# Optimization experiments

Hardware: AMD Instinct MI355X
Metric: run time of the kernel (lower is better)

The kernel has to match this reference:

```python
import jax, jax.numpy as jnp
import numpy as np

N_HEADS = 16
HEAD_DIM = 64
D_MODEL = N_HEADS * HEAD_DIM
NEG_INF = -10000.0


def setup_inputs() -> dict:
    key = jax.random.key(0)
    ks = jax.random.split(key, 6)
    B, S = 2, 2048
    std = 0.02
    return {
        "from_tensor": jax.random.normal(ks[0], (B, S, D_MODEL), dtype=jnp.float32),
        "to_tensor": jax.random.normal(ks[1], (B, S, D_MODEL), dtype=jnp.float32),
        "attention_mask": jnp.ones((B, S, S), dtype=jnp.int32),
        "Wq": jax.random.normal(ks[2], (D_MODEL, D_MODEL), dtype=jnp.float32) * std,
        "bq": jnp.zeros((D_MODEL,), dtype=jnp.float32),
        "Wk": jax.random.normal(ks[3], (D_MODEL, D_MODEL), dtype=jnp.float32) * std,
        "bk": jnp.zeros((D_MODEL,), dtype=jnp.float32),
        "Wv": jax.random.normal(ks[4], (D_MODEL, D_MODEL), dtype=jnp.float32) * std,
        "bv": jnp.zeros((D_MODEL,), dtype=jnp.float32),
    }


def reference(from_tensor, to_tensor, attention_mask, Wq, bq, Wk, bk, Wv, bv):
    B, F, _ = from_tensor.shape
    T = to_tensor.shape[1]
    # Dense QKV projections (no activation by default)
    q = from_tensor @ Wq + bq          # [B, F, N*H]
    k = to_tensor @ Wk + bk            # [B, T, N*H]
    v = to_tensor @ Wv + bv            # [B, T, N*H]
    # split heads -> [B, N, S, H]
    q = q.reshape(B, F, N_HEADS, HEAD_DIM).transpose(0, 2, 1, 3)
    k = k.reshape(B, T, N_HEADS, HEAD_DIM).transpose(0, 2, 1, 3)
    v = v.reshape(B, T, N_HEADS, HEAD_DIM).transpose(0, 2, 1, 3)
    # scaled dot-product scores [B, N, F, T]
    scores = jnp.einsum("bnfh,bnth->bnft", q, k) / jnp.sqrt(jnp.float32(HEAD_DIM))
    # additive mask: (1 - mask) * -10000, broadcast over heads
    adder = (1.0 - attention_mask.astype(jnp.float32))[:, None, :, :] * NEG_INF
    scores = scores + adder
    probs = jax.nn.softmax(scores, axis=-1)  # dropout is identity at inference
    ctx = jnp.einsum("bnft,bnth->bnfh", probs, v)  # [B, N, F, H]
    return ctx.transpose(0, 2, 1, 3).reshape(B, F, N_HEADS * HEAD_DIM)
```

## Files before the change

### kernel.cpp

```cpp
#include <hip/hip_runtime.h>
#include <hip/hip_bf16.h>

typedef unsigned short u16;
typedef __bf16 bf16x8 __attribute__((ext_vector_type(8)));
typedef float f32x4 __attribute__((ext_vector_type(4)));

#define D_MODEL 1024
#define NH 16
#define HD 64
#define SEQ 2048
#define BATCH 2

__device__ __forceinline__ f32x4 mfma16(bf16x8 a, bf16x8 b, f32x4 c) {
    return __builtin_amdgcn_mfma_f32_16x16x32_bf16(a, b, c, 0, 0, 0);
}

__device__ __forceinline__ u16 f2bf(float f) {
    __hip_bfloat16 h = __float2bfloat16(f);
    return *reinterpret_cast<u16*>(&h);
}

__device__ __forceinline__ void gload_lds16(const void* g, void* l) {
    __builtin_amdgcn_global_load_lds((__attribute__((address_space(1))) void*)g,
                                     (__attribute__((address_space(3))) void*)l,
                                     16, 0, 0);
}

__global__ __launch_bounds__(256) void convert_k(const float* __restrict__ src,
                                                 u16* __restrict__ dst, int n8) {
    const int i = blockIdx.x * 256 + threadIdx.x;
    if (i >= n8) return;
    const float4 a = ((const float4*)src)[i * 2];
    const float4 b = ((const float4*)src)[i * 2 + 1];
    union { u16 h[8]; uint4 v; } u;
    u.h[0] = f2bf(a.x); u.h[1] = f2bf(a.y); u.h[2] = f2bf(a.z); u.h[3] = f2bf(a.w);
    u.h[4] = f2bf(b.x); u.h[5] = f2bf(b.y); u.h[6] = f2bf(b.z); u.h[7] = f2bf(b.w);
    *(uint4*)(dst + i * 8) = u.v;
}

__global__ __launch_bounds__(256) void transposeW_k(const float* __restrict__ src,
                                                    u16* __restrict__ dst,
                                                    int R, int C) {
    __shared__ __align__(16) u16 t[64][72];
    const int tid = threadIdx.x;
    const int r0 = blockIdx.y * 64, c0 = blockIdx.x * 64;
#pragma unroll
    for (int j = 0; j < 2; ++j) {
        int idx = j * 256 + tid;
        int rr = idx >> 3, cc = idx & 7;
        size_t base = (size_t)(r0 + rr) * C + c0 + cc * 8;
        float4 a = *(const float4*)(src + base);
        float4 b = *(const float4*)(src + base + 4);
        union { u16 h[8]; uint4 v; } u;
        u.h[0] = f2bf(a.x); u.h[1] = f2bf(a.y); u.h[2] = f2bf(a.z); u.h[3] = f2bf(a.w);
        u.h[4] = f2bf(b.x); u.h[5] = f2bf(b.y); u.h[6] = f2bf(b.z); u.h[7] = f2bf(b.w);
        *(uint4*)&t[rr][cc * 8] = u.v;
    }
    __syncthreads();
#pragma unroll
    for (int j = 0; j < 2; ++j) {
        int idx = j * 256 + tid;
        int cc = idx >> 3, rr8 = idx & 7;
        union { u16 h[8]; uint4 v; } u;
#pragma unroll
        for (int e = 0; e < 8; ++e) u.h[e] = t[rr8 * 8 + e][cc];
        *(uint4*)(dst + (size_t)(c0 + cc) * R + r0 + rr8 * 8) = u.v;
    }
}

__global__ __launch_bounds__(256) void maskflags_k(const int* __restrict__ mask,
                                                   int* __restrict__ flags) {
    const int tid = threadIdx.x;
    const int ti = blockIdx.x, fi = blockIdx.y, b = blockIdx.z;
    const int f = fi * 128 + (tid >> 1);
    const int4* p = (const int4*)(mask + ((size_t)(b * SEQ + f)) * SEQ + ti * 64 + (tid & 1) * 32);
    int ok = 1;
#pragma unroll
    for (int j = 0; j < 8; ++j) {
        int4 v = p[j];
        ok &= (v.x == 1) & (v.y == 1) & (v.z == 1) & (v.w == 1);
    }
    __shared__ int sflag;
    if (tid == 0) sflag = 1;
    __syncthreads();
    if (!ok) sflag = 0;
    __syncthreads();
    if (tid == 0) flags[(b * 16 + fi) * 32 + ti] = sflag;
}

__global__ __launch_bounds__(256, 2) void qkv_gemm_k(
    const u16* __restrict__ Xq, const u16* __restrict__ Xkv,
    const u16* __restrict__ Wt,
    const float* __restrict__ bq, const float* __restrict__ bk,
    const float* __restrict__ bv,
    u16* __restrict__ Qb, u16* __restrict__ Kb, u16* __restrict__ Vt) {
    const int z = blockIdx.z;
    const u16* X = (z == 0) ? Xq : Xkv;
    const u16* Wz = Wt + (size_t)z * D_MODEL * D_MODEL;
    const float* bias = (z == 0) ? bq : (z == 1 ? bk : bv);
    const float scale = (z == 0) ? 0.1803368801111244f : 1.0f;

    __shared__ __align__(16) u16 As[128 * 32];
    __shared__ __align__(16) u16 Bs[128 * 32];

    const int tid = threadIdx.x;
    const int w = tid >> 6, lane = tid & 63;
    const int q = lane >> 4, c = lane & 15;
    const int m0 = blockIdx.x * 128, n0 = blockIdx.y * 128;
    const int mw = (w & 1) * 64, nw = (w >> 1) * 64;

    f32x4 acc[4][4];
    const f32x4 z4 = {0.f, 0.f, 0.f, 0.f};
#pragma unroll
    for (int mi = 0; mi < 4; ++mi)
#pragma unroll
        for (int ni = 0; ni < 4; ++ni) acc[mi][ni] = z4;

    for (int kb = 0; kb < 32; ++kb) {
        const int k0 = kb * 32;
#pragma unroll
        for (int j = 0; j < 2; ++j) {
            int i = j * 256 + tid;
            int r = i >> 2, cc = i & 3;
            gload_lds16(X + (size_t)(m0 + r) * D_MODEL + k0 + cc * 8, As + i * 8);
            gload_lds16(Wz + (size_t)(n0 + r) * D_MODEL + k0 + cc * 8, Bs + i * 8);
        }
        __syncthreads();
        bf16x8 af[4], bfr[4];
#pragma unroll
        for (int mi = 0; mi < 4; ++mi)
            af[mi] = *(const bf16x8*)(As + (mw + mi * 16 + c) * 32 + q * 8);
#pragma unroll
        for (int ni = 0; ni < 4; ++ni)
            bfr[ni] = *(const bf16x8*)(Bs + (nw + ni * 16 + c) * 32 + q * 8);
#pragma unroll
        for (int mi = 0; mi < 4; ++mi)
#pragma unroll
            for (int ni = 0; ni < 4; ++ni)
                acc[mi][ni] = mfma16(af[mi], bfr[ni], acc[mi][ni]);
        __syncthreads();
    }

    if (z == 2) {
#pragma unroll
        for (int ni = 0; ni < 4; ++ni) {
            const int colg = n0 + nw + ni * 16 + c;
            const float bvv = bias[colg];
            const int head = colg >> 6, h = colg & 63;
#pragma unroll
            for (int mi = 0; mi < 4; ++mi) {
                const int rowg = m0 + mw + mi * 16 + q * 4;
                const int b = rowg >> 11, s = rowg & 2047;
                union { u16 h4[4]; uint2 v2; } pk;
#pragma unroll
                for (int r = 0; r < 4; ++r) pk.h4[r] = f2bf(acc[mi][ni][r] + bvv);
                *(uint2*)(Vt + (((size_t)(b * NH + head)) * HD + h) * SEQ + s) = pk.v2;
            }
        }
    } else {
        u16* outb = (z == 0) ? Qb : Kb;
#pragma unroll
        for (int ni = 0; ni < 4; ++ni) {
            const int colg = n0 + nw + ni * 16 + c;
            const float bvv = bias[colg];
            const int head = colg >> 6, h = colg & 63;
#pragma unroll
            for (int mi = 0; mi < 4; ++mi) {
                const int rowg = m0 + mw + mi * 16 + q * 4;
#pragma unroll
                for (int r = 0; r < 4; ++r) {
                    const int mrow = rowg + r;
                    const int b = mrow >> 11, s = mrow & 2047;
                    const float val = (acc[mi][ni][r] + bvv) * scale;
                    outb[(((size_t)(b * NH + head)) * SEQ + s) * HD + h] = f2bf(val);
                }
            }
        }
    }
}

#define SK_OFF (128 * 144)
#define SV_OFF (SK_OFF + 64 * 144)
#define SMEM_BYTES (SV_OFF + 64 * 144)

__global__ __launch_bounds__(256, 4) void attn_k(
    const u16* __restrict__ Qb, const u16* __restrict__ Kb, const u16* __restrict__ Vt,
    const int* __restrict__ flags, const int* __restrict__ mask,
    float* __restrict__ out) {
    __shared__ __align__(16) unsigned char smem[SMEM_BYTES];
    const int tid = threadIdx.x;
    const int w = tid >> 6, lane = tid & 63;
    const int q = lane >> 4, c = lane & 15;
    const int fi = blockIdx.x, bn = blockIdx.y;
    const int b = bn >> 4, n = bn & 15;
    const int f0 = fi * 128;

    u16* sQ = (u16*)(smem);
    u16* sK = (u16*)(smem + SK_OFF);
    u16* sV = (u16*)(smem + SV_OFF);
    u16* sP = sQ + w * 32 * 72;

#pragma unroll
    for (int j = 0; j < 4; ++j) {
        int i = j * 256 + tid;
        int r = i >> 3, cc = i & 7;
        uint4 v = *(const uint4*)(Qb + ((size_t)(bn * SEQ + f0 + r)) * HD + cc * 8);
        *(uint4*)(sQ + r * 72 + cc * 8) = v;
    }
    __syncthreads();

    bf16x8 qf[2][2];
#pragma unroll
    for (int ft = 0; ft < 2; ++ft)
#pragma unroll
        for (int kb = 0; kb < 2; ++kb)
            qf[ft][kb] = *(const bf16x8*)(sQ + (w * 32 + ft * 16 + c) * 72 + kb * 32 + q * 8);
    __asm__ __volatile__("" ::: "memory");
    __builtin_amdgcn_s_waitcnt(0xC07F);
    __asm__ __volatile__("" ::: "memory");

    union { u16 h[8]; bf16x8 v; } one_u;
#pragma unroll
    for (int j = 0; j < 8; ++j) one_u.h[j] = 0x3F80;
    const bf16x8 ones = one_u.v;

    f32x4 O[2][4], accL[2];
    const f32x4 z4 = {0.f, 0.f, 0.f, 0.f};
#pragma unroll
    for (int mi = 0; mi < 2; ++mi) {
        accL[mi] = z4;
#pragma unroll
        for (int hi = 0; hi < 4; ++hi) O[mi][hi] = z4;
    }
    const int* flagp = flags + (b * 16 + fi) * 32;

    for (int it = 0; it < 32; ++it) {
        const int t0 = it * 64;
#pragma unroll
        for (int j = 0; j < 2; ++j) {
            int i = j * 256 + tid;
            int r = i >> 3, cc = i & 7;
            uint4 kv = *(const uint4*)(Kb + ((size_t)(bn * SEQ + t0 + r)) * HD + cc * 8);
            uint4 vv = *(const uint4*)(Vt + ((size_t)(bn * HD + r)) * SEQ + t0 + cc * 8);
            *(uint4*)(sK + r * 72 + cc * 8) = kv;
            *(uint4*)(sV + r * 72 + cc * 8) = vv;
        }
        __syncthreads();

        const int maskslow = (flagp[it] == 0);

#pragma unroll
        for (int mt = 0; mt < 4; ++mt) {
            bf16x8 kf0 = *(const bf16x8*)(sK + (mt * 16 + c) * 72 + 0 + q * 8);
            bf16x8 kf1 = *(const bf16x8*)(sK + (mt * 16 + c) * 72 + 32 + q * 8);
            f32x4 st[2];
#pragma unroll
            for (int ft = 0; ft < 2; ++ft) {
                st[ft] = z4;
                st[ft] = mfma16(kf0, qf[ft][0], st[ft]);
                st[ft] = mfma16(kf1, qf[ft][1], st[ft]);
            }
            if (maskslow) {
#pragma unroll
                for (int ft = 0; ft < 2; ++ft)
#pragma unroll
                    for (int r = 0; r < 4; ++r) {
                        const int fg = f0 + w * 32 + ft * 16 + c;
                        const int tg = t0 + mt * 16 + q * 4 + r;
                        const int mv = mask[((size_t)(b * SEQ + fg)) * SEQ + tg];
                        st[ft][r] += (1.0f - (float)mv) * (-10000.0f) * 1.4426950408889634f;
                    }
            }
#pragma unroll
            for (int ft = 0; ft < 2; ++ft) {
                union { u16 h[4]; uint2 v2; } pk;
#pragma unroll
                for (int r = 0; r < 4; ++r)
                    pk.h[r] = f2bf(exp2f(st[ft][r] - 10.0f));
                *(uint2*)(sP + (ft * 16 + c) * 72 + mt * 16 + q * 4) = pk.v2;
            }
        }
        __asm__ __volatile__("" ::: "memory");
        __builtin_amdgcn_s_waitcnt(0xC07F);
        __asm__ __volatile__("" ::: "memory");

#pragma unroll
        for (int kb = 0; kb < 2; ++kb) {
            bf16x8 pf0 = *(const bf16x8*)(sP + (0 * 16 + c) * 72 + kb * 32 + q * 8);
            bf16x8 pf1 = *(const bf16x8*)(sP + (1 * 16 + c) * 72 + kb * 32 + q * 8);
#pragma unroll
            for (int hi = 0; hi < 4; ++hi) {
                bf16x8 vf = *(const bf16x8*)(sV + (hi * 16 + c) * 72 + kb * 32 + q * 8);
                O[0][hi] = mfma16(pf0, vf, O[0][hi]);
                O[1][hi] = mfma16(pf1, vf, O[1][hi]);
            }
            accL[0] = mfma16(pf0, ones, accL[0]);
            accL[1] = mfma16(pf1, ones, accL[1]);
        }
        __syncthreads();
    }

    float linv[2][4];
#pragma unroll
    for (int mi = 0; mi < 2; ++mi)
#pragma unroll
        for (int r = 0; r < 4; ++r) linv[mi][r] = 1.0f / accL[mi][r];
#pragma unroll
    for (int mi = 0; mi < 2; ++mi)
#pragma unroll
        for (int hi = 0; hi < 4; ++hi)
#pragma unroll
            for (int r = 0; r < 4; ++r) {
                const int fg = f0 + w * 32 + mi * 16 + q * 4 + r;
                const int col = n * 64 + hi * 16 + c;
                out[((size_t)(b * SEQ + fg)) * D_MODEL + col] = O[mi][hi][r] * linv[mi][r];
            }
}

__global__ __launch_bounds__(256) void signal_k(float* __restrict__ out, int n,
                                                float val) {
    const int i = blockIdx.x * 256 + threadIdx.x;
    if (i < n) out[i] = val;
}

extern "C" void kernel_launch(void* const* d_in, const int* in_sizes, int n_in,
                              void* d_out, int out_size, void* d_ws, size_t ws_size,
                              hipStream_t stream) {
    const float* Xs[2] = {nullptr, nullptr};
    const float* Wp[3] = {nullptr, nullptr, nullptr};
    const float* Bp[3] = {nullptr, nullptr, nullptr};
    const int* mask = nullptr;
    int nx = 0, nw = 0, nb = 0;
    for (int i = 0; i < n_in; ++i) {
        const long long sz = in_sizes[i];
        if (sz == (long long)BATCH * SEQ * D_MODEL) {
            if (nx < 2) Xs[nx++] = (const float*)d_in[i];
        } else if (sz == (long long)BATCH * SEQ * SEQ) {
            mask = (const int*)d_in[i];
        } else if (sz == (long long)D_MODEL * D_MODEL) {
            if (nw < 3) Wp[nw++] = (const float*)d_in[i];
        } else if (sz == (long long)D_MODEL) {
            if (nb < 3) Bp[nb++] = (const float*)d_in[i];
        }
    }
    float* outp = (float*)d_out;
    const size_t MB = 1024 * 1024;
    const size_t NEED = 47 * MB;

    if (ws_size < NEED || nx != 2 || nw != 3 || nb != 3 || !mask) {
        float code = 1000.0f + (float)(ws_size / MB)
                   + (nx != 2 ? 10000.0f : 0.f)
                   + (nw != 3 ? 20000.0f : 0.f)
                   + (nb != 3 ? 40000.0f : 0.f)
                   + (!mask   ? 80000.0f : 0.f);
        signal_k<<<(out_size + 255) / 256, 256, 0, stream>>>(outp, out_size, code);
        return;
    }

    char* ws = (char*)d_ws;
    u16* Xqc   = (u16*)(ws);
    u16* Xkvc  = (u16*)(ws + 8 * MB);
    u16* Wt    = (u16*)(ws + 16 * MB);
    u16* Qb    = (u16*)(ws + 22 * MB);
    u16* Kb    = (u16*)(ws + 30 * MB);
    u16* Vt    = (u16*)(ws + 38 * MB);
    int* flags = (int*)(ws + 46 * MB);

    convert_k<<<2048, 256, 0, stream>>>(Xs[0], Xqc, 524288);
    convert_k<<<2048, 256, 0, stream>>>(Xs[1], Xkvc, 524288);
    transposeW_k<<<dim3(16, 16), 256, 0, stream>>>(Wp[0], Wt,               1024, 1024);
    transposeW_k<<<dim3(16, 16), 256, 0, stream>>>(Wp[1], Wt + 1024 * 1024, 1024, 1024);
    transposeW_k<<<dim3(16, 16), 256, 0, stream>>>(Wp[2], Wt + 2048 * 1024, 1024, 1024);
    maskflags_k<<<dim3(32, 16, 2), 256, 0, stream>>>(mask, flags);
    qkv_gemm_k<<<dim3(32, 8, 3), 256, 0, stream>>>(Xqc, Xkvc, Wt,
                                                   Bp[0], Bp[1], Bp[2], Qb, Kb, Vt);
    attn_k<<<dim3(16, 32), 256, 0, stream>>>(Qb, Kb, Vt, flags, mask, outp);
}
```

Measured before the change: 237.9 us.

## Halve attention query tile to 64 rows and double grid size

Reduces the query rows per attention block from 128 to 64, giving each wave 16 rows and doubling the number of blocks. P gets a dedicated LDS region instead of aliasing Q. This is meant to increase occupancy and CU coverage. In exchange, K/V tiles are loaded twice as often per query row, per-wave MFMA reuse of K/V fragments drops, and an extra block barrier is added per iteration.

```diff
diff --git a/kernel.cpp b/kernel.cpp
--- a/kernel.cpp
+++ b/kernel.cpp
@@ -179,9 +179,10 @@
     }
 }
 
-#define SK_OFF (128 * 144)
+#define SK_OFF (64 * 144)
 #define SV_OFF (SK_OFF + 64 * 144)
-#define SMEM_BYTES (SV_OFF + 64 * 144)
+#define SP_OFF (SV_OFF + 64 * 144)
+#define SMEM_BYTES (SP_OFF + 64 * 144)
 
 __global__ __launch_bounds__(256, 4) void attn_k(
     const u16* __restrict__ Qb, const u16* __restrict__ Kb, const u16* __restrict__ Vt,
@@ -193,15 +194,15 @@
     const int q = lane >> 4, c = lane & 15;
     const int fi = blockIdx.x, bn = blockIdx.y;
     const int b = bn >> 4, n = bn & 15;
-    const int f0 = fi * 128;
+    const int f0 = fi * 64;
 
     u16* sQ = (u16*)(smem);
     u16* sK = (u16*)(smem + SK_OFF);
     u16* sV = (u16*)(smem + SV_OFF);
-    u16* sP = sQ + w * 32 * 72;
-
-#pragma unroll
-    for (int j = 0; j < 4; ++j) {
+    u16* sP = (u16*)(smem + SP_OFF) + w * 16 * 72;
+
+#pragma unroll
+    for (int j = 0; j < 2; ++j) {
         int i = j * 256 + tid;
         int r = i >> 3, cc = i & 7;
         uint4 v = *(const uint4*)(Qb + ((size_t)(bn * SEQ + f0 + r)) * HD + cc * 8);
@@ -209,30 +210,23 @@
     }
     __syncthreads();
 
-    bf16x8 qf[2][2];
-#pragma unroll
-    for (int ft = 0; ft < 2; ++ft)
-#pragma unroll
-        for (int kb = 0; kb < 2; ++kb)
-            qf[ft][kb] = *(const bf16x8*)(sQ + (w * 32 + ft * 16 + c) * 72 + kb * 32 + q * 8);
-    __asm__ __volatile__("" ::: "memory");
-    __builtin_amdgcn_s_waitcnt(0xC07F);
-    __asm__ __volatile__("" ::: "memory");
+    bf16x8 qf[2];
+#pragma unroll
+    for (int kb = 0; kb < 2; ++kb)
+        qf[kb] = *(const bf16x8*)(sQ + (w * 16 + c) * 72 + kb * 32 + q * 8);
 
     union { u16 h[8]; bf16x8 v; } one_u;
 #pragma unroll
     for (int j = 0; j < 8; ++j) one_u.h[j] = 0x3F80;
     const bf16x8 ones = one_u.v;
 
-    f32x4 O[2][4], accL[2];
+    f32x4 O[4], accL;
     const f32x4 z4 = {0.f, 0.f, 0.f, 0.f};
-#pragma unroll
-    for (int mi = 0; mi < 2; ++mi) {
-        accL[mi] = z4;
-#pragma unroll
-        for (int hi = 0; hi < 4; ++hi) O[mi][hi] = z4;
-    }
-    const int* flagp = flags + (b * 16 + fi) * 32;
+    accL = z4;
+#pragma unroll
+    for (int hi = 0; hi < 4; ++hi) O[hi] = z4;
+
+    const int* flagp = flags + (b * 16 + (fi >> 1)) * 32;
 
     for (int it = 0; it < 32; ++it) {
         const int t0 = it * 64;
@@ -253,68 +247,50 @@
         for (int mt = 0; mt < 4; ++mt) {
             bf16x8 kf0 = *(const bf16x8*)(sK + (mt * 16 + c) * 72 + 0 + q * 8);
             bf16x8 kf1 = *(const bf16x8*)(sK + (mt * 16 + c) * 72 + 32 + q * 8);
-            f32x4 st[2];
-#pragma unroll
-            for (int ft = 0; ft < 2; ++ft) {
-                st[ft] = z4;
-                st[ft] = mfma16(kf0, qf[ft][0], st[ft]);
-                st[ft] = mfma16(kf1, qf[ft][1], st[ft]);
+            f32x4 st = z4;
+            st = mfma16(kf0, qf[0], st);
+            st = mfma16(kf1, qf[1], st);
+            if (maskslow) {
+#pragma unroll
+                for (int r = 0; r < 4; ++r) {
+                    const int fg = f0 + w * 16 + c;
+                    const int tg = t0 + mt * 16 + q * 4 + r;
+                    const int mv = mask[((size_t)(b * SEQ + fg)) * SEQ + tg];
+                    st[r] += (1.0f - (float)mv) * (-10000.0f) * 1.4426950408889634f;
+                }
             }
-            if (maskslow) {
-#pragma unroll
-                for (int ft = 0; ft < 2; ++ft)
-#pragma unroll
-                    for (int r = 0; r < 4; ++r) {
-                        const int fg = f0 + w * 32 + ft * 16 + c;
-                        const int tg = t0 + mt * 16 + q * 4 + r;
-                        const int mv = mask[((size_t)(b * SEQ + fg)) * SEQ + tg];
-                        st[ft][r] += (1.0f - (float)mv) * (-10000.0f) * 1.4426950408889634f;
-                    }
-            }
-#pragma unroll
-            for (int ft = 0; ft < 2; ++ft) {
-                union { u16 h[4]; uint2 v2; } pk;
-#pragma unroll
-                for (int r = 0; r < 4; ++r)
-                    pk.h[r] = f2bf(exp2f(st[ft][r] - 10.0f));
-                *(uint2*)(sP + (ft * 16 + c) * 72 + mt * 16 + q * 4) = pk.v2;
-            }
-        }
-        __asm__ __volatile__("" ::: "memory");
-        __builtin_amdgcn_s_waitcnt(0xC07F);
-        __asm__ __volatile__("" ::: "memory");
+            union { u16 h[4]; uint2 v2; } pk;
+#pragma unroll
+            for (int r = 0; r < 4; ++r)
+                pk.h[r] = f2bf(exp2f(st[r] - 10.0f));
+            *(uint2*)(sP + c * 72 + mt * 16 + q * 4) = pk.v2;
+        }
+        __syncthreads();
 
 #pragma unroll
         for (int kb = 0; kb < 2; ++kb) {
-            bf16x8 pf0 = *(const bf16x8*)(sP + (0 * 16 + c) * 72 + kb * 32 + q * 8);
-            bf16x8 pf1 = *(const bf16x8*)(sP + (1 * 16 + c) * 72 + kb * 32 + q * 8);
+            bf16x8 pf = *(const bf16x8*)(sP + c * 72 + kb * 32 + q * 8);
 #pragma unroll
             for (int hi = 0; hi < 4; ++hi) {
                 bf16x8 vf = *(const bf16x8*)(sV + (hi * 16 + c) * 72 + kb * 32 + q * 8);
-                O[0][hi] = mfma16(pf0, vf, O[0][hi]);
-                O[1][hi] = mfma16(pf1, vf, O[1][hi]);
+                O[hi] = mfma16(pf, vf, O[hi]);
             }
-            accL[0] = mfma16(pf0, ones, accL[0]);
-            accL[1] = mfma16(pf1, ones, accL[1]);
-        }
-        __syncthreads();
-    }
-
-    float linv[2][4];
-#pragma unroll
-    for (int mi = 0; mi < 2; ++mi)
-#pragma unroll
-        for (int r = 0; r < 4; ++r) linv[mi][r] = 1.0f / accL[mi][r];
-#pragma unroll
-    for (int mi = 0; mi < 2; ++mi)
-#pragma unroll
-        for (int hi = 0; hi < 4; ++hi)
-#pragma unroll
-            for (int r = 0; r < 4; ++r) {
-                const int fg = f0 + w * 32 + mi * 16 + q * 4 + r;
-                const int col = n * 64 + hi * 16 + c;
-                out[((size_t)(b * SEQ + fg)) * D_MODEL + col] = O[mi][hi][r] * linv[mi][r];
-            }
+            accL = mfma16(pf, ones, accL);
+        }
+        __syncthreads();
+    }
+
+    float linv[4];
+#pragma unroll
+    for (int r = 0; r < 4; ++r) linv[r] = 1.0f / accL[r];
+#pragma unroll
+    for (int hi = 0; hi < 4; ++hi)
+#pragma unroll
+        for (int r = 0; r < 4; ++r) {
+            const int fg = f0 + w * 16 + q * 4 + r;
+            const int col = n * 64 + hi * 16 + c;
+            out[((size_t)(b * SEQ + fg)) * D_MODEL + col] = O[hi][r] * linv[r];
+        }
 }
 
 __global__ __launch_bounds__(256) void signal_k(float* __restrict__ out, int n,
@@ -374,5 +350,5 @@
     maskflags_k<<<dim3(32, 16, 2), 256, 0, stream>>>(mask, flags);
     qkv_gemm_k<<<dim3(32, 8, 3), 256, 0, stream>>>(Xqc, Xkvc, Wt,
                                                    Bp[0], Bp[1], Bp[2], Qb, Kb, Vt);
-    attn_k<<<dim3(16, 32), 256, 0, stream>>>(Qb, Kb, Vt, flags, mask, outp);
-}
+    attn_k<<<dim3(32, 32), 256, 0, stream>>>(Qb, Kb, Vt, flags, mask, outp);
+}
```

New measurement: 239.2 us. No clear change (+0.5%).

## Split attention key range across two blocks and combine partial results

Applied to the files above, without the earlier changes.

Adds a z-dimension of two to the attention grid, so each block processes half of the key sequence. Each block writes unnormalized partial outputs and row sums to workspace, and a new combine kernel adds the two halves and normalizes them. This doubles the block count so more CUs stay busy. In exchange it writes and rereads an extra full fp32 output buffer and adds one more kernel launch. The split is exact only because the softmax here uses no running-max rescale.

```diff
diff --git a/kernel.cpp b/kernel.cpp
--- a/kernel.cpp
+++ b/kernel.cpp
@@ -186,12 +186,13 @@
 __global__ __launch_bounds__(256, 4) void attn_k(
     const u16* __restrict__ Qb, const u16* __restrict__ Kb, const u16* __restrict__ Vt,
     const int* __restrict__ flags, const int* __restrict__ mask,
+    float* __restrict__ O0, float* __restrict__ l0, float* __restrict__ l1,
     float* __restrict__ out) {
     __shared__ __align__(16) unsigned char smem[SMEM_BYTES];
     const int tid = threadIdx.x;
     const int w = tid >> 6, lane = tid & 63;
     const int q = lane >> 4, c = lane & 15;
-    const int fi = blockIdx.x, bn = blockIdx.y;
+    const int fi = blockIdx.x, bn = blockIdx.y, ts = blockIdx.z;
     const int b = bn >> 4, n = bn & 15;
     const int f0 = fi * 128;
 
@@ -234,7 +235,8 @@
     }
     const int* flagp = flags + (b * 16 + fi) * 32;
 
-    for (int it = 0; it < 32; ++it) {
+    const int it0 = ts * 16;
+    for (int it = it0; it < it0 + 16; ++it) {
         const int t0 = it * 64;
 #pragma unroll
         for (int j = 0; j < 2; ++j) {
@@ -300,11 +302,8 @@
         __syncthreads();
     }
 
-    float linv[2][4];
-#pragma unroll
-    for (int mi = 0; mi < 2; ++mi)
-#pragma unroll
-        for (int r = 0; r < 4; ++r) linv[mi][r] = 1.0f / accL[mi][r];
+    float* Odst = ts ? out : O0;
+    float* ldst = ts ? l1 : l0;
 #pragma unroll
     for (int mi = 0; mi < 2; ++mi)
 #pragma unroll
@@ -313,8 +312,37 @@
             for (int r = 0; r < 4; ++r) {
                 const int fg = f0 + w * 32 + mi * 16 + q * 4 + r;
                 const int col = n * 64 + hi * 16 + c;
-                out[((size_t)(b * SEQ + fg)) * D_MODEL + col] = O[mi][hi][r] * linv[mi][r];
-            }
+                Odst[((size_t)(b * SEQ + fg)) * D_MODEL + col] = O[mi][hi][r];
+            }
+    if (c == 0) {
+#pragma unroll
+        for (int mi = 0; mi < 2; ++mi)
+#pragma unroll
+            for (int r = 0; r < 4; ++r) {
+                const int fg = f0 + w * 32 + mi * 16 + q * 4 + r;
+                ldst[(size_t)bn * SEQ + fg] = accL[mi][r];
+            }
+    }
+}
+
+__global__ __launch_bounds__(256) void combine_k(const float* __restrict__ O0,
+                                                 const float* __restrict__ l0,
+                                                 const float* __restrict__ l1,
+                                                 float* __restrict__ out) {
+    const int i = blockIdx.x * 256 + threadIdx.x;
+    const int bf = i >> 8;
+    const int col = (i & 255) << 2;
+    const int n = col >> 6;
+    const int lidx = ((bf >> 11) * NH + n) * SEQ + (bf & (SEQ - 1));
+    const float inv = 1.0f / (l0[lidx] + l1[lidx]);
+    const float4 a = ((const float4*)O0)[i];
+    const float4 cpart = ((const float4*)out)[i];
+    float4 r;
+    r.x = (a.x + cpart.x) * inv;
+    r.y = (a.y + cpart.y) * inv;
+    r.z = (a.z + cpart.z) * inv;
+    r.w = (a.w + cpart.w) * inv;
+    ((float4*)out)[i] = r;
 }
 
 __global__ __launch_bounds__(256) void signal_k(float* __restrict__ out, int n,
@@ -365,6 +393,9 @@
     u16* Kb    = (u16*)(ws + 30 * MB);
     u16* Vt    = (u16*)(ws + 38 * MB);
     int* flags = (int*)(ws + 46 * MB);
+    float* O0 = (float*)(ws);
+    float* l0 = (float*)(ws + 46 * MB + 16 * 1024);
+    float* l1 = (float*)(ws + 46 * MB + 16 * 1024 + 256 * 1024);
 
     convert_k<<<2048, 256, 0, stream>>>(Xs[0], Xqc, 524288);
     convert_k<<<2048, 256, 0, stream>>>(Xs[1], Xkvc, 524288);
@@ -374,5 +405,7 @@
     maskflags_k<<<dim3(32, 16, 2), 256, 0, stream>>>(mask, flags);
     qkv_gemm_k<<<dim3(32, 8, 3), 256, 0, stream>>>(Xqc, Xkvc, Wt,
                                                    Bp[0], Bp[1], Bp[2], Qb, Kb, Vt);
-    attn_k<<<dim3(16, 32), 256, 0, stream>>>(Qb, Kb, Vt, flags, mask, outp);
-}
+    attn_k<<<dim3(16, 32, 2), 256, 0, stream>>>(Qb, Kb, Vt, flags, mask,
+                                                O0, l0, l1, outp);
+    combine_k<<<4096, 256, 0, stream>>>(O0, l0, l1, outp);
+}
```

Measured after the change: 232.8 us. 1.02x faster.
